# Optimization experiments

Hardware: AMD Instinct MI355X
Metric: run time of the kernel (lower is better)

Reference implementation:

```python
import jax, jax.numpy as jnp
import numpy as np

NUM_CLASSES = 1000
BATCH = 65536
TEMPERATURE = 1.0
SMOOTHING = 0.1


def setup_inputs() -> dict:
    key = jax.random.key(0)
    k1, k2, k3 = jax.random.split(key, 3)
    x = jax.random.normal(k1, (BATCH, NUM_CLASSES), dtype=jnp.float32)
    class_avg = jax.random.normal(k2, (NUM_CLASSES, NUM_CLASSES), dtype=jnp.float32)
    target = jax.random.randint(k3, (BATCH,), 0, NUM_CLASSES, dtype=jnp.int64)
    return {"x": x, "class_avg": class_avg, "target": target}


def reference(x, class_avg, target):
    C = class_avg.shape[0]
    # class_avg = softmax(class_avg / T) over last dim
    A = jax.nn.softmax(class_avg / TEMPERATURE, axis=-1)  # [C, C]
    # per-class off-diagonal mass: sum over row minus diagonal
    sums = A.sum(axis=-1) - jnp.diagonal(A)  # [C]
    # per-class smoothing matrix S[t, j] = smoothing * (1 - A[t, j]) / sums[t], S[t, t] = 1 - smoothing
    S = SMOOTHING * (1.0 - A) / sums[:, None]  # [C, C]
    diag_idx = jnp.arange(C)
    S = S.at[diag_idx, diag_idx].set(1.0 - SMOOTHING)
    # gather the per-sample smoothing rows (replaces the nested Python loop)
    sm = S[target]  # [B, C]
    logprobs = jax.nn.log_softmax(x, axis=-1)  # [B, C]
    loss = -(logprobs * sm).sum(axis=-1)  # [B]
    return loss.mean()
```

## Files before the change

kernel.cpp:

```cpp
#include <hip/hip_runtime.h>
#include <hip/hip_bf16.h>
#include <math.h>

constexpr int C = 1000;
constexpr int B = 65536;
constexpr float SMOOTH = 0.1f;

__device__ inline float wave_reduce_max(float v) {
    #pragma unroll
    for (int off = 32; off > 0; off >>= 1)
        v = fmaxf(v, __shfl_xor(v, off, 64));
    return v;
}
__device__ inline float wave_reduce_sum(float v) {
    #pragma unroll
    for (int off = 32; off > 0; off >>= 1)
        v += __shfl_xor(v, off, 64);
    return v;
}

__device__ inline float block_reduce_max(float v, float* sm) {
    v = wave_reduce_max(v);
    int wave = threadIdx.x >> 6, lane = threadIdx.x & 63;
    if (lane == 0) sm[wave] = v;
    __syncthreads();
    float r = fmaxf(fmaxf(sm[0], sm[1]), fmaxf(sm[2], sm[3]));
    __syncthreads();
    return r;
}
__device__ inline float block_reduce_sum(float v, float* sm) {
    v = wave_reduce_sum(v);
    int wave = threadIdx.x >> 6, lane = threadIdx.x & 63;
    if (lane == 0) sm[wave] = v;
    __syncthreads();
    float r = sm[0] + sm[1] + sm[2] + sm[3];
    __syncthreads();
    return r;
}

__global__ __launch_bounds__(256) void smooth_kernel(
        const float* __restrict__ ca, float* __restrict__ S,
        float* __restrict__ Srow) {
    __shared__ float sm[4];
    __shared__ float diag_sh;
    int t = blockIdx.x;
    int tid = threadIdx.x;
    const float* row = ca + (size_t)t * C;

    float v[4];
    float m = -INFINITY;
    #pragma unroll
    for (int k = 0; k < 4; k++) {
        int j = tid + k * 256;
        v[k] = (j < C) ? row[j] : -INFINITY;
        m = fmaxf(m, v[k]);
    }
    m = block_reduce_max(m, sm);

    float a[4];
    float zl = 0.f;
    #pragma unroll
    for (int k = 0; k < 4; k++) {
        int j = tid + k * 256;
        a[k] = (j < C) ? __expf(v[k] - m) : 0.f;
        zl += a[k];
    }
    float z = block_reduce_sum(zl, sm);
    float inv_z = 1.0f / z;

    float sumA_l = 0.f;
    #pragma unroll
    for (int k = 0; k < 4; k++) {
        a[k] *= inv_z;
        sumA_l += a[k];
        int j = tid + k * 256;
        if (j == t) diag_sh = a[k];
    }
    float sumA = block_reduce_sum(sumA_l, sm);

    float sums = sumA - diag_sh;
    float coef = SMOOTH / sums;
    float* Srt = S + (size_t)t * C;
    float srow_l = 0.f;
    #pragma unroll
    for (int k = 0; k < 4; k++) {
        int j = tid + k * 256;
        if (j < C) {
            float s = (j == t) ? (1.0f - SMOOTH) : (1.0f - a[k]) * coef;
            Srt[j] = s;
            srow_l += s;
        }
    }
    float srow = block_reduce_sum(srow_l, sm);
    if (tid == 0) Srow[t] = srow;
}

__global__ __launch_bounds__(256) void loss_kernel(
        const float* __restrict__ x, const float* __restrict__ S,
        const float* __restrict__ Srow, const int* __restrict__ tgt,
        float* __restrict__ out) {
    int wave = threadIdx.x >> 6, lane = threadIdx.x & 63;
    int wgid = blockIdx.x * 4 + wave;
    int nw = gridDim.x * 4;
    float acc = 0.f;

    for (int b = wgid; b < B; b += nw) {
        int t = tgt[b];
        const float4* xr = (const float4*)(x + (size_t)b * C);
        const float4* sr = (const float4*)(S + (size_t)t * C);
        float4 xv[4], sv[4];
        #pragma unroll
        for (int k = 0; k < 3; k++) {
            xv[k] = xr[lane + k * 64];
            sv[k] = sr[lane + k * 64];
        }
        bool last = (lane + 192) < 250;
        if (last) {
            xv[3] = xr[lane + 192];
            sv[3] = sr[lane + 192];
        } else {
            xv[3] = make_float4(-INFINITY, -INFINITY, -INFINITY, -INFINITY);
            sv[3] = make_float4(0.f, 0.f, 0.f, 0.f);
        }

        float m = -INFINITY;
        #pragma unroll
        for (int k = 0; k < 4; k++)
            m = fmaxf(m, fmaxf(fmaxf(xv[k].x, xv[k].y), fmaxf(xv[k].z, xv[k].w)));
        m = wave_reduce_max(m);

        float zl = 0.f, dl = 0.f;
        #pragma unroll
        for (int k = 0; k < 4; k++) {
            zl += __expf(xv[k].x - m) + __expf(xv[k].y - m) +
                  __expf(xv[k].z - m) + __expf(xv[k].w - m);
        }
        #pragma unroll
        for (int k = 0; k < 3; k++) {
            dl = fmaf(sv[k].x, xv[k].x, dl);
            dl = fmaf(sv[k].y, xv[k].y, dl);
            dl = fmaf(sv[k].z, xv[k].z, dl);
            dl = fmaf(sv[k].w, xv[k].w, dl);
        }
        if (last) {
            dl = fmaf(sv[3].x, xv[3].x, dl);
            dl = fmaf(sv[3].y, xv[3].y, dl);
            dl = fmaf(sv[3].z, xv[3].z, dl);
            dl = fmaf(sv[3].w, xv[3].w, dl);
        }
        float z = wave_reduce_sum(zl);
        float d = wave_reduce_sum(dl);
        float ss = Srow[t];
        float lb = (m + __logf(z)) * ss - d;
        acc += lb;
    }

    __shared__ float wacc[4];
    if (lane == 0) wacc[wave] = acc;
    __syncthreads();
    if (threadIdx.x == 0) {
        float tot = wacc[0] + wacc[1] + wacc[2] + wacc[3];
        atomicAdd(out, tot * (1.0f / (float)B));
    }
}

extern "C" void kernel_launch(void* const* d_in, const int* in_sizes, int n_in,
                              void* d_out, int out_size, void* d_ws, size_t ws_size,
                              hipStream_t stream) {
    const float* x   = (const float*)d_in[0];
    const float* ca  = (const float*)d_in[1];
    const int*   tgt = (const int*)d_in[2];
    float* out = (float*)d_out;

    float* S    = (float*)d_ws;
    float* Srow = S + (size_t)C * C;

    hipMemsetAsync(out, 0, sizeof(float), stream);
    smooth_kernel<<<C, 256, 0, stream>>>(ca, S, Srow);
    loss_kernel<<<4096, 256, 0, stream>>>(x, S, Srow, tgt, out);
}
```

Measured before the change: 367.8 us.

## Use one row per wave, nontemporal x loads, and deterministic partial reduction

```diff
diff --git a/kernel.cpp b/kernel.cpp
--- a/kernel.cpp
+++ b/kernel.cpp
@@ -5,6 +5,9 @@
 constexpr int C = 1000;
 constexpr int B = 65536;
 constexpr float SMOOTH = 0.1f;
+constexpr int NBLK = B / 4;
+
+typedef float f4 __attribute__((ext_vector_type(4)));
 
 __device__ inline float wave_reduce_max(float v) {
     #pragma unroll
@@ -98,70 +101,78 @@
 __global__ __launch_bounds__(256) void loss_kernel(
         const float* __restrict__ x, const float* __restrict__ S,
         const float* __restrict__ Srow, const int* __restrict__ tgt,
-        float* __restrict__ out) {
+        float* __restrict__ partials) {
     int wave = threadIdx.x >> 6, lane = threadIdx.x & 63;
-    int wgid = blockIdx.x * 4 + wave;
-    int nw = gridDim.x * 4;
-    float acc = 0.f;
+    int b = blockIdx.x * 4 + wave;
 
-    for (int b = wgid; b < B; b += nw) {
-        int t = tgt[b];
-        const float4* xr = (const float4*)(x + (size_t)b * C);
-        const float4* sr = (const float4*)(S + (size_t)t * C);
-        float4 xv[4], sv[4];
-        #pragma unroll
-        for (int k = 0; k < 3; k++) {
-            xv[k] = xr[lane + k * 64];
-            sv[k] = sr[lane + k * 64];
-        }
-        bool last = (lane + 192) < 250;
-        if (last) {
-            xv[3] = xr[lane + 192];
-            sv[3] = sr[lane + 192];
-        } else {
-            xv[3] = make_float4(-INFINITY, -INFINITY, -INFINITY, -INFINITY);
-            sv[3] = make_float4(0.f, 0.f, 0.f, 0.f);
-        }
+    int t = tgt[b];
+    float ss = Srow[t];
+    const f4* xr = (const f4*)(x + (size_t)b * C);
+    const f4* sr = (const f4*)(S + (size_t)t * C);
 
-        float m = -INFINITY;
-        #pragma unroll
-        for (int k = 0; k < 4; k++)
-            m = fmaxf(m, fmaxf(fmaxf(xv[k].x, xv[k].y), fmaxf(xv[k].z, xv[k].w)));
-        m = wave_reduce_max(m);
-
-        float zl = 0.f, dl = 0.f;
-        #pragma unroll
-        for (int k = 0; k < 4; k++) {
-            zl += __expf(xv[k].x - m) + __expf(xv[k].y - m) +
-                  __expf(xv[k].z - m) + __expf(xv[k].w - m);
-        }
-        #pragma unroll
-        for (int k = 0; k < 3; k++) {
-            dl = fmaf(sv[k].x, xv[k].x, dl);
-            dl = fmaf(sv[k].y, xv[k].y, dl);
-            dl = fmaf(sv[k].z, xv[k].z, dl);
-            dl = fmaf(sv[k].w, xv[k].w, dl);
-        }
-        if (last) {
-            dl = fmaf(sv[3].x, xv[3].x, dl);
-            dl = fmaf(sv[3].y, xv[3].y, dl);
-            dl = fmaf(sv[3].z, xv[3].z, dl);
-            dl = fmaf(sv[3].w, xv[3].w, dl);
-        }
-        float z = wave_reduce_sum(zl);
-        float d = wave_reduce_sum(dl);
-        float ss = Srow[t];
-        float lb = (m + __logf(z)) * ss - d;
-        acc += lb;
+    f4 xv[4], sv[4];
+    #pragma unroll
+    for (int k = 0; k < 3; k++) {
+        xv[k] = __builtin_nontemporal_load(xr + lane + k * 64);
+        sv[k] = sr[lane + k * 64];
+    }
+    bool last = (lane + 192) < 250;
+    if (last) {
+        xv[3] = __builtin_nontemporal_load(xr + lane + 192);
+        sv[3] = sr[lane + 192];
+    } else {
+        xv[3] = f4{-INFINITY, -INFINITY, -INFINITY, -INFINITY};
+        sv[3] = f4{0.f, 0.f, 0.f, 0.f};
     }
 
+    float m = -INFINITY;
+    #pragma unroll
+    for (int k = 0; k < 4; k++)
+        m = fmaxf(m, fmaxf(fmaxf(xv[k].x, xv[k].y), fmaxf(xv[k].z, xv[k].w)));
+    m = wave_reduce_max(m);
+
+    float zl = 0.f, dl = 0.f;
+    #pragma unroll
+    for (int k = 0; k < 4; k++) {
+        zl += __expf(xv[k].x - m) + __expf(xv[k].y - m) +
+              __expf(xv[k].z - m) + __expf(xv[k].w - m);
+    }
+    #pragma unroll
+    for (int k = 0; k < 3; k++) {
+        dl = fmaf(sv[k].x, xv[k].x, dl);
+        dl = fmaf(sv[k].y, xv[k].y, dl);
+        dl = fmaf(sv[k].z, xv[k].z, dl);
+        dl = fmaf(sv[k].w, xv[k].w, dl);
+    }
+    if (last) {
+        dl = fmaf(sv[3].x, xv[3].x, dl);
+        dl = fmaf(sv[3].y, xv[3].y, dl);
+        dl = fmaf(sv[3].z, xv[3].z, dl);
+        dl = fmaf(sv[3].w, xv[3].w, dl);
+    }
+    float z = wave_reduce_sum(zl);
+    float d = wave_reduce_sum(dl);
+    float lb = (m + __logf(z)) * ss - d;
+
     __shared__ float wacc[4];
-    if (lane == 0) wacc[wave] = acc;
+    if (lane == 0) wacc[wave] = lb;
     __syncthreads();
-    if (threadIdx.x == 0) {
-        float tot = wacc[0] + wacc[1] + wacc[2] + wacc[3];
-        atomicAdd(out, tot * (1.0f / (float)B));
+    if (threadIdx.x == 0)
+        partials[blockIdx.x] = wacc[0] + wacc[1] + wacc[2] + wacc[3];
+}
+
+__global__ __launch_bounds__(256) void reduce_kernel(
+        const float* __restrict__ partials, float* __restrict__ out) {
+    __shared__ float sm[4];
+    const f4* p4 = (const f4*)partials;
+    float s = 0.f;
+    #pragma unroll
+    for (int k = 0; k < 16; k++) {
+        f4 v = p4[threadIdx.x + k * 256];
+        s += (v.x + v.y) + (v.z + v.w);
     }
+    s = block_reduce_sum(s, sm);
+    if (threadIdx.x == 0) out[0] = s * (1.0f / (float)B);
 }
 
 extern "C" void kernel_launch(void* const* d_in, const int* in_sizes, int n_in,
@@ -172,10 +183,11 @@
     const int*   tgt = (const int*)d_in[2];
     float* out = (float*)d_out;
 
-    float* S    = (float*)d_ws;
-    float* Srow = S + (size_t)C * C;
+    float* S        = (float*)d_ws;
+    float* Srow     = S + (size_t)C * C;
+    float* partials = Srow + C;
 
-    hipMemsetAsync(out, 0, sizeof(float), stream);
     smooth_kernel<<<C, 256, 0, stream>>>(ca, S, Srow);
-    loss_kernel<<<4096, 256, 0, stream>>>(x, S, Srow, tgt, out);
+    loss_kernel<<<NBLK, 256, 0, stream>>>(x, S, Srow, tgt, partials);
+    reduce_kernel<<<1, 256, 0, stream>>>(partials, out);
 }
```

Measured after the change: 342.3 us. 6.9% less time.
